# Kernel tuning notes

Measured on AMD Instinct MI355X. Metric: run time of the kernel, lower is better.

## Reference

```python
import jax, jax.numpy as jnp
import numpy as np

N = 50000   # nodes
E = 640000  # edges
D_IN = 128
D_OUT = 128
EPS = 1e-5


def _layer_norm(x, gamma, beta):
    mu = jnp.mean(x, axis=-1, keepdims=True)
    var = jnp.mean(jnp.square(x - mu), axis=-1, keepdims=True)
    return (x - mu) * jax.lax.rsqrt(var + EPS) * gamma + beta


def _sage_conv(x, src, dst, w_l, b_l, w_r):
    # PyG SAGEConv (aggr='mean', root_weight=True, normalize=False):
    #   out = lin_l(mean_{j in N(i)} x_j) + lin_r(x_i)
    msgs = x[src]                                             # [E, D]
    agg = jax.ops.segment_sum(msgs, dst, num_segments=N)      # [N, D]
    cnt = jax.ops.segment_sum(jnp.ones((E,), x.dtype), dst, num_segments=N)
    mean = agg / jnp.maximum(cnt, 1.0)[:, None]
    return mean @ w_l.T + b_l + x @ w_r.T


def setup_inputs() -> dict:
    key = jax.random.key(0)
    ks = jax.random.split(key, 12)
    s_in = 1.0 / np.sqrt(D_IN)
    s_out = 1.0 / np.sqrt(D_OUT)
    return {
        "x": jax.random.normal(ks[0], (N, D_IN), jnp.float32),
        "edges": jax.random.randint(ks[1], (2, E), 0, N),
        "dp_w": jax.random.uniform(ks[2], (D_OUT, D_IN), jnp.float32, -s_in, s_in),
        "dp_b": jnp.zeros((D_OUT,), jnp.float32),
        "sc_w": jax.random.uniform(ks[3], (D_OUT, D_IN), jnp.float32, -s_in, s_in),
        "sc_b": jnp.zeros((D_OUT,), jnp.float32),
        "g1_lw": jax.random.uniform(ks[4], (D_OUT, D_OUT), jnp.float32, -s_out, s_out),
        "g1_lb": jnp.zeros((D_OUT,), jnp.float32),
        "g1_rw": jax.random.uniform(ks[5], (D_OUT, D_OUT), jnp.float32, -s_out, s_out),
        "n1_g": jnp.ones((D_OUT,), jnp.float32),
        "n1_b": jnp.zeros((D_OUT,), jnp.float32),
        "g2_lw": jax.random.uniform(ks[6], (D_OUT, D_OUT), jnp.float32, -s_out, s_out),
        "g2_lb": jnp.zeros((D_OUT,), jnp.float32),
        "g2_rw": jax.random.uniform(ks[7], (D_OUT, D_OUT), jnp.float32, -s_out, s_out),
        "n2_g": jnp.ones((D_OUT,), jnp.float32),
        "n2_b": jnp.zeros((D_OUT,), jnp.float32),
    }


def reference(x, edges, dp_w, dp_b, sc_w, sc_b, g1_lw, g1_lb, g1_rw, n1_g, n1_b,
              g2_lw, g2_lb, g2_rw, n2_g, n2_b):
    gelu = lambda v: jax.nn.gelu(v, approximate=False)
    src, dst = edges[0], edges[1]
    shortcut = x @ sc_w.T + sc_b
    h = gelu(x @ dp_w.T + dp_b)
    h = _sage_conv(h, src, dst, g1_lw, g1_lb, g1_rw)
    h = gelu(_layer_norm(h, n1_g, n1_b))
    h = _sage_conv(h, src, dst, g2_lw, g2_lb, g2_rw)
    h = _layer_norm(h, n2_g, n2_b)
    return gelu(h + shortcut)
```

## Files before the change

kernel.cpp:

```cpp
#include <hip/hip_runtime.h>
#include <hip/hip_bf16.h>
#include <math.h>

#define D 128
#define WS 136
#define FS 132
#define PB 128

typedef __attribute__((ext_vector_type(8))) short bf16x8;
typedef __attribute__((ext_vector_type(4))) float f32x4;

__device__ __forceinline__ unsigned short f2bf(float f){
  return (unsigned short)((__float_as_uint(f) + 0x8000u) >> 16);
}
__device__ __forceinline__ float bf2f(unsigned short h){
  return __uint_as_float(((unsigned)h) << 16);
}
__device__ __forceinline__ float bf2f_lo(unsigned v){
  return __uint_as_float(v << 16);
}
__device__ __forceinline__ float bf2f_hi(unsigned v){
  return __uint_as_float(v & 0xFFFF0000u);
}
__device__ __forceinline__ float gelu_fast(float v){
  float u = v * v;
  float arg = v * (1.5957691216f + 0.0713548163f * u);
  arg = fminf(arg, 60.0f);
  float e = __expf(arg);
  return v * e * __builtin_amdgcn_rcpf(e + 1.0f);
}

__global__ __launch_bounds__(256) void k_prepcnt(const float* s0, const float* s1,
    const float* s2, const float* s3, const float* s4, const float* s5,
    unsigned short* dst, const int* __restrict__ edst, int* __restrict__ cnt,
    int E, int nbuck, int epb){
  __shared__ int hist[512];
  if (blockIdx.x < 48){
    int gt = blockIdx.x * 256 + threadIdx.x;
    int m = gt >> 11;
    int r = gt & 2047;
    int f = r >> 6, lane = r & 63;
    int t = f & 7, kk = f >> 3;
    int row = t * 16 + (lane & 15);
    int col = kk * 32 + (lane >> 4) * 8;
    const float* src;
    if (m == 0) src = s0; else if (m == 1) src = s1; else if (m == 2) src = s2;
    else if (m == 3) src = s3; else if (m == 4) src = s4; else src = s5;
    src += row * 128 + col;
    float4 a = *(const float4*)src;
    float4 bb = *(const float4*)(src + 4);
    bf16x8 o;
    o[0] = (short)f2bf(a.x);  o[1] = (short)f2bf(a.y);
    o[2] = (short)f2bf(a.z);  o[3] = (short)f2bf(a.w);
    o[4] = (short)f2bf(bb.x); o[5] = (short)f2bf(bb.y);
    o[6] = (short)f2bf(bb.z); o[7] = (short)f2bf(bb.w);
    int pair = m >> 1, half = m & 1;
    *(bf16x8*)(dst + (size_t)pair * 32768 + (((size_t)f * 2 + half) * 64 + lane) * 8) = o;
    return;
  }
  int blk = blockIdx.x - 48;
  for (int b = threadIdx.x; b < nbuck; b += 256) hist[b] = 0;
  __syncthreads();
  int start = blk * epb;
  int end = min(E, start + epb);
  for (int e = start + threadIdx.x; e < end; e += 256)
    atomicAdd(&hist[edst[e] >> 7], 1);
  __syncthreads();
  for (int b = threadIdx.x; b < nbuck; b += 256) cnt[blk * nbuck + b] = hist[b];
}

__global__ __launch_bounds__(128) void k_scanA(const int* __restrict__ cnt,
    int* __restrict__ offs_rel, int* __restrict__ tot, int nbuck){
  __shared__ int sm[128];
  int b = blockIdx.x, t = threadIdx.x;
  int v = cnt[t * nbuck + b];
  sm[t] = v; __syncthreads();
  for (int ofs = 1; ofs < 128; ofs <<= 1){
    int u = (t >= ofs) ? sm[t - ofs] : 0;
    __syncthreads();
    sm[t] += u;
    __syncthreads();
  }
  offs_rel[t * nbuck + b] = sm[t] - v;
  if (t == 127) tot[b] = sm[127];
}

__global__ __launch_bounds__(256) void k_pscatter(const int* __restrict__ esrc,
    const int* __restrict__ edst, const int* __restrict__ offs_rel,
    const int* __restrict__ tot, unsigned* __restrict__ ebuf,
    int E, int nbuck, int epb){
  __shared__ int stot[512];
  __shared__ int loff[512];
  for (int b = threadIdx.x; b < nbuck; b += 256) stot[b] = tot[b];
  __syncthreads();
  for (int b = threadIdx.x; b < nbuck; b += 256){
    int s = 0;
    for (int j = 0; j < b; j++) s += stot[j];
    loff[b] = s + offs_rel[blockIdx.x * nbuck + b];
  }
  __syncthreads();
  int start = blockIdx.x * epb;
  int end = min(E, start + epb);
  for (int e = start + threadIdx.x; e < end; e += 256){
    int s = esrc[e], d = edst[e];
    int b = d >> 7;
    int pos = atomicAdd(&loff[b], 1);
    ebuf[pos] = (unsigned)s | ((unsigned)(d & 127) << 16);
  }
}

__global__ __launch_bounds__(256) void k_csrin(
    const unsigned* __restrict__ ebuf, const int* __restrict__ tot,
    int* __restrict__ off, int* __restrict__ csr,
    const float* __restrict__ x, const unsigned short* __restrict__ wp,
    const float* __restrict__ scb, const float* __restrict__ dpb,
    unsigned short* __restrict__ sbuf, unsigned short* __restrict__ hbuf,
    int N, int E, int nbuck){
  __shared__ int cnt[128], pref[128], curs[128];
  __shared__ int stot[512], red[256];
  __shared__ unsigned short tile[64 * WS];
  int tid = threadIdx.x;
  if ((int)blockIdx.x < nbuck){
    int b = blockIdx.x;
    for (int j = tid; j < nbuck; j += 256) stot[j] = tot[j];
    __syncthreads();
    int part = 0;
    for (int j = tid; j < b; j += 256) part += stot[j];
    red[tid] = part;
    __syncthreads();
    for (int ofs = 128; ofs > 0; ofs >>= 1){
      if (tid < ofs) red[tid] += red[tid + ofs];
      __syncthreads();
    }
    int start = red[0];
    int end = start + stot[b];
    if (tid < 128) cnt[tid] = 0;
    __syncthreads();
    for (int e = start + tid; e < end; e += 256)
      atomicAdd(&cnt[ebuf[e] >> 16], 1);
    __syncthreads();
    if (tid < 128) pref[tid] = cnt[tid];
    __syncthreads();
    for (int ofs = 1; ofs < 128; ofs <<= 1){
      int v = 0;
      if (tid < 128 && tid >= ofs) v = pref[tid - ofs];
      __syncthreads();
      if (tid < 128) pref[tid] += v;
      __syncthreads();
    }
    if (tid < 128){
      int ex = pref[tid] - cnt[tid];
      curs[tid] = ex;
      int node = b * 128 + tid;
      if (node < N) off[node] = start + ex;
    }
    if (b == 0 && tid == 0) off[N] = E;
    __syncthreads();
    for (int e = start + tid; e < end; e += 256){
      unsigned u = ebuf[e];
      int d = u >> 16;
      int p = atomicAdd(&curs[d], 1);
      csr[start + p] = (int)(u & 0xFFFFu);
    }
    return;
  }
  int bx = blockIdx.x - nbuck;
  int w = tid >> 6, lane = tid & 63, quad = lane >> 4, l16 = lane & 15;
  int nbb = bx * 64;
  int nb = nbb + w * 16;
  int arow = min(nb + l16, N - 1);
  f32x4 acc[2][8];
  #pragma unroll
  for (int m = 0; m < 2; m++)
    #pragma unroll
    for (int t = 0; t < 8; t++) acc[m][t] = (f32x4){0.f, 0.f, 0.f, 0.f};
  #pragma unroll
  for (int kk = 0; kk < 4; kk++){
    const float* xp = x + (size_t)arow * D + kk * 32 + quad * 8;
    float4 xa = *(const float4*)xp;
    float4 xb = *(const float4*)(xp + 4);
    bf16x8 a;
    a[0] = (short)f2bf(xa.x); a[1] = (short)f2bf(xa.y);
    a[2] = (short)f2bf(xa.z); a[3] = (short)f2bf(xa.w);
    a[4] = (short)f2bf(xb.x); a[5] = (short)f2bf(xb.y);
    a[6] = (short)f2bf(xb.z); a[7] = (short)f2bf(xb.w);
    #pragma unroll
    for (int t = 0; t < 8; t++){
      size_t fo = (((size_t)(kk * 8 + t) * 2) * 64 + lane) * 8;
      bf16x8 b0 = *(const bf16x8*)(wp + fo);
      bf16x8 b1 = *(const bf16x8*)(wp + fo + 512);
      acc[0][t] = __builtin_amdgcn_mfma_f32_16x16x32_bf16(a, b0, acc[0][t], 0, 0, 0);
      acc[1][t] = __builtin_amdgcn_mfma_f32_16x16x32_bf16(a, b1, acc[1][t], 0, 0, 0);
    }
  }
  #pragma unroll
  for (int m = 0; m < 2; m++){
    const float* bias = m ? dpb : scb;
    #pragma unroll
    for (int t = 0; t < 8; t++){
      float bv = bias[t * 16 + l16];
      #pragma unroll
      for (int r = 0; r < 4; r++){
        int nl = w * 16 + quad * 4 + r;
        float v = acc[m][t][r] + bv;
        if (m) v = gelu_fast(v);
        tile[nl * WS + t * 16 + l16] = f2bf(v);
      }
    }
    __syncthreads();
    unsigned short* dst = m ? hbuf : sbuf;
    #pragma unroll
    for (int i = 0; i < 4; i++){
      int c = tid + 256 * i;
      int nl = c >> 4, j = c & 15;
      int node = nbb + nl;
      if (node < N)
        *(bf16x8*)(dst + (size_t)node * D + j * 8) = *(const bf16x8*)(tile + nl * WS + j * 8);
    }
    __syncthreads();
  }
}

__global__ __launch_bounds__(256) void k_gall(
    const unsigned short* __restrict__ hin,
    const int* __restrict__ off, const int* __restrict__ csr,
    const unsigned short* __restrict__ wp,
    const float* __restrict__ lb, const float* __restrict__ gamma,
    const float* __restrict__ beta,
    const unsigned short* __restrict__ sbuf,
    unsigned short* __restrict__ hout, float* __restrict__ fout, int N, int mode){
  extern __shared__ char smraw[];
  unsigned short* mtile = (unsigned short*)smraw;
  unsigned short* stile = (unsigned short*)smraw;
  float* ftile = (float*)smraw;
  int tid = threadIdx.x;
  int nbb = blockIdx.x * 64;
  {
    int q = tid >> 4, l16g = tid & 15;
    int n0 = nbb + q * 4;
    int s0 = off[min(n0 + 0, N)];
    int s1 = off[min(n0 + 1, N)];
    int s2 = off[min(n0 + 2, N)];
    int s3 = off[min(n0 + 3, N)];
    int s4 = off[min(n0 + 4, N)];
    float aT[8], a1[8], a2[8], a3[8];
    #pragma unroll
    for (int c = 0; c < 8; c++){ aT[c] = 0.f; a1[c] = 0.f; a2[c] = 0.f; a3[c] = 0.f; }
    if (s4 > s0){
      int nn[8];
      #pragma unroll
      for (int i = 0; i < 8; i++) nn[i] = csr[min(s0 + i, s4 - 1)];
      for (int e = s0; e < s4; e += 8){
        uint4 v[8];
        #pragma unroll
        for (int i = 0; i < 8; i++)
          v[i] = *(const uint4*)(hin + (size_t)nn[i] * D + l16g * 8);
        #pragma unroll
        for (int i = 0; i < 8; i++) nn[i] = csr[min(e + 8 + i, s4 - 1)];
        #pragma unroll
        for (int i = 0; i < 8; i++){
          int ei = e + i;
          float mT = (ei < s4) ? 1.f : 0.f;
          float m1 = (ei >= s1) ? mT : 0.f;
          float m2 = (ei >= s2) ? mT : 0.f;
          float m3 = (ei >= s3) ? mT : 0.f;
          float fv[8];
          fv[0] = bf2f_lo(v[i].x); fv[1] = bf2f_hi(v[i].x);
          fv[2] = bf2f_lo(v[i].y); fv[3] = bf2f_hi(v[i].y);
          fv[4] = bf2f_lo(v[i].z); fv[5] = bf2f_hi(v[i].z);
          fv[6] = bf2f_lo(v[i].w); fv[7] = bf2f_hi(v[i].w);
          #pragma unroll
          for (int c = 0; c < 8; c++){
            aT[c] += mT * fv[c];
            a1[c] += m1 * fv[c];
            a2[c] += m2 * fv[c];
            a3[c] += m3 * fv[c];
          }
        }
      }
    }
    float i0 = 1.f / (float)max(s1 - s0, 1);
    float i1 = 1.f / (float)max(s2 - s1, 1);
    float i2 = 1.f / (float)max(s3 - s2, 1);
    float i3 = 1.f / (float)max(s4 - s3, 1);
    bf16x8 o0, o1, o2, o3;
    #pragma unroll
    for (int c = 0; c < 8; c++){
      o0[c] = (short)f2bf((aT[c] - a1[c]) * i0);
      o1[c] = (short)f2bf((a1[c] - a2[c]) * i1);
      o2[c] = (short)f2bf((a2[c] - a3[c]) * i2);
      o3[c] = (short)f2bf(a3[c] * i3);
    }
    *(bf16x8*)(mtile + (q * 4 + 0) * WS + l16g * 8) = o0;
    *(bf16x8*)(mtile + (q * 4 + 1) * WS + l16g * 8) = o1;
    *(bf16x8*)(mtile + (q * 4 + 2) * WS + l16g * 8) = o2;
    *(bf16x8*)(mtile + (q * 4 + 3) * WS + l16g * 8) = o3;
  }
  __syncthreads();
  int w = tid >> 6, lane = tid & 63, quad = lane >> 4, l16 = lane & 15;
  int nb = nbb + w * 16;
  int arow = min(nb + l16, N - 1);
  int mrow = w * 16 + l16;
  bf16x8 am[4], ah[4];
  #pragma unroll
  for (int kk = 0; kk < 4; kk++){
    am[kk] = *(const bf16x8*)(mtile + mrow * WS + kk * 32 + quad * 8);
    ah[kk] = *(const bf16x8*)(hin + (size_t)arow * D + kk * 32 + quad * 8);
  }
  f32x4 acc[8];
  #pragma unroll
  for (int t = 0; t < 8; t++) acc[t] = (f32x4){0.f, 0.f, 0.f, 0.f};
  #pragma unroll
  for (int kk = 0; kk < 4; kk++){
    #pragma unroll
    for (int t = 0; t < 8; t++){
      size_t fo = (((size_t)(kk * 8 + t) * 2) * 64 + lane) * 8;
      bf16x8 bl = *(const bf16x8*)(wp + fo);
      bf16x8 br = *(const bf16x8*)(wp + fo + 512);
      acc[t] = __builtin_amdgcn_mfma_f32_16x16x32_bf16(am[kk], bl, acc[t], 0, 0, 0);
      acc[t] = __builtin_amdgcn_mfma_f32_16x16x32_bf16(ah[kk], br, acc[t], 0, 0, 0);
    }
  }
  float lbv[8], gv[8], bv[8];
  #pragma unroll
  for (int t = 0; t < 8; t++){
    lbv[t] = lb[t * 16 + l16];
    gv[t] = gamma[t * 16 + l16];
    bv[t] = beta[t * 16 + l16];
  }
  float mu[4], rs[4];
  #pragma unroll
  for (int r = 0; r < 4; r++){
    float s = 0.f, qq = 0.f;
    #pragma unroll
    for (int t = 0; t < 8; t++){
      float v = acc[t][r] + lbv[t];
      acc[t][r] = v;
      s += v; qq += v * v;
    }
    s += __shfl_xor(s, 1); qq += __shfl_xor(qq, 1);
    s += __shfl_xor(s, 2); qq += __shfl_xor(qq, 2);
    s += __shfl_xor(s, 4); qq += __shfl_xor(qq, 4);
    s += __shfl_xor(s, 8); qq += __shfl_xor(qq, 8);
    float m_ = s * (1.f / 128.f);
    mu[r] = m_;
    rs[r] = rsqrtf(qq * (1.f / 128.f) - m_ * m_ + 1e-5f);
  }
  __syncthreads();
  if (mode == 0){
    #pragma unroll
    for (int t = 0; t < 8; t++)
      #pragma unroll
      for (int r = 0; r < 4; r++){
        int nl = w * 16 + quad * 4 + r;
        float v = (acc[t][r] - mu[r]) * rs[r] * gv[t] + bv[t];
        stile[nl * WS + t * 16 + l16] = f2bf(gelu_fast(v));
      }
    __syncthreads();
    #pragma unroll
    for (int i = 0; i < 4; i++){
      int c = tid + 256 * i;
      int nl = c >> 4, j = c & 15;
      int node = nbb + nl;
      if (node < N)
        *(bf16x8*)(hout + (size_t)node * D + j * 8) = *(const bf16x8*)(stile + nl * WS + j * 8);
    }
  } else {
    #pragma unroll
    for (int i = 0; i < 4; i++){
      int c = tid + 256 * i;
      int nl = c >> 4, j = c & 15;
      int node = nbb + nl;
      bf16x8 v = (bf16x8){0,0,0,0,0,0,0,0};
      if (node < N) v = *(const bf16x8*)(sbuf + (size_t)node * D + j * 8);
      *(bf16x8*)(stile + nl * WS + j * 8) = v;
    }
    __syncthreads();
    float sc[8][4];
    #pragma unroll
    for (int t = 0; t < 8; t++)
      #pragma unroll
      for (int r = 0; r < 4; r++){
        int nl = w * 16 + quad * 4 + r;
        sc[t][r] = bf2f(stile[nl * WS + t * 16 + l16]);
      }
    __syncthreads();
    #pragma unroll
    for (int t = 0; t < 8; t++)
      #pragma unroll
      for (int r = 0; r < 4; r++){
        int nl = w * 16 + quad * 4 + r;
        float v = (acc[t][r] - mu[r]) * rs[r] * gv[t] + bv[t];
        ftile[nl * FS + t * 16 + l16] = gelu_fast(v + sc[t][r]);
      }
    __syncthreads();
    #pragma unroll
    for (int i = 0; i < 8; i++){
      int c = tid + 256 * i;
      int nl = c >> 5, j = c & 31;
      int node = nbb + nl;
      if (node < N)
        *(float4*)(fout + (size_t)node * D + j * 4) = *(const float4*)(ftile + nl * FS + j * 4);
    }
  }
}

extern "C" void kernel_launch(void* const* d_in, const int* in_sizes, int n_in,
                              void* d_out, int out_size, void* d_ws, size_t ws_size,
                              hipStream_t stream){
  const float* x     = (const float*)d_in[0];
  const int*   edges = (const int*)d_in[1];
  const float* dp_w  = (const float*)d_in[2];
  const float* dp_b  = (const float*)d_in[3];
  const float* sc_w  = (const float*)d_in[4];
  const float* sc_b  = (const float*)d_in[5];
  const float* g1_lw = (const float*)d_in[6];
  const float* g1_lb = (const float*)d_in[7];
  const float* g1_rw = (const float*)d_in[8];
  const float* n1_g  = (const float*)d_in[9];
  const float* n1_b  = (const float*)d_in[10];
  const float* g2_lw = (const float*)d_in[11];
  const float* g2_lb = (const float*)d_in[12];
  const float* g2_rw = (const float*)d_in[13];
  const float* n2_g  = (const float*)d_in[14];
  const float* n2_b  = (const float*)d_in[15];

  const int N = in_sizes[0] / D;
  const int E = in_sizes[1] / 2;
  const int* esrc = edges;
  const int* edst = edges + E;
  const int nbuck = (N + 127) >> 7;
  const int epb = (E + PB - 1) / PB;

  char* base = (char*)d_ws;
  size_t cur = 0;
  auto carve = [&](size_t b) -> char* {
    char* p = base + cur;
    cur = (cur + b + 255) & ~(size_t)255;
    return p;
  };
  unsigned* ebuf  = (unsigned*)carve((size_t)E * 4);
  int* cnt        = (int*)carve((size_t)PB * nbuck * 4);
  int* offs_rel   = (int*)carve((size_t)PB * nbuck * 4);
  int* tot        = (int*)carve((size_t)nbuck * 4);
  int* off        = (int*)carve((size_t)(N + 1) * 4);
  int* csr        = (int*)carve((size_t)E * 4);
  unsigned short* wb    = (unsigned short*)carve((size_t)3 * 32768 * 2);
  unsigned short* hbuf  = (unsigned short*)carve((size_t)N * D * 2);
  unsigned short* h1buf = (unsigned short*)carve((size_t)N * D * 2);
  unsigned short* sbuf  = (unsigned short*)carve((size_t)N * D * 2);

  unsigned short* wp0 = wb;
  unsigned short* wp1 = wb + 32768;
  unsigned short* wp2 = wb + 2 * 32768;

  float* out = (float*)d_out;

  k_prepcnt<<<48 + PB, 256, 0, stream>>>(sc_w, dp_w, g1_lw, g1_rw, g2_lw, g2_rw,
                                         wb, edst, cnt, E, nbuck, epb);
  k_scanA<<<nbuck, 128, 0, stream>>>(cnt, offs_rel, tot, nbuck);
  k_pscatter<<<PB, 256, 0, stream>>>(esrc, edst, offs_rel, tot, ebuf, E, nbuck, epb);

  const int nin = (N + 63) / 64;
  k_csrin<<<nbuck + nin, 256, 0, stream>>>(ebuf, tot, off, csr,
                                           x, wp0, sc_b, dp_b, sbuf, hbuf,
                                           N, E, nbuck);

  k_gall<<<nin, 256, 17408, stream>>>(hbuf, off, csr, wp1, g1_lb, n1_g, n1_b,
                                      nullptr, h1buf, nullptr, N, 0);
  k_gall<<<nin, 256, 33792, stream>>>(h1buf, off, csr, wp2, g2_lb, n2_g, n2_b,
                                      sbuf, nullptr, out, N, 1);
}
```

Before: 231.5 us.

## Split fused gather+GEMM into separate per-node gather and GEMM kernels

Splits the fused neighbor-mean aggregation and MFMA GEMM kernel into two kernels. The gather now assigns 16 lanes per node, one node per group, with no masked 4-node accumulation. It writes the mean to a new global bf16 buffer that the GEMM kernel then reads. This removes the redundant four-accumulator masked work and the load imbalance of the fused gather, and adds parallelism. The cost is an extra global round trip of an N×128 bf16 buffer and two extra kernel launches.

```diff
diff --git a/kernel.cpp b/kernel.cpp
--- a/kernel.cpp
+++ b/kernel.cpp
@@ -221,90 +221,71 @@
   }
 }
 
-__global__ __launch_bounds__(256) void k_gall(
+__global__ __launch_bounds__(256) void k_gather(
     const unsigned short* __restrict__ hin,
     const int* __restrict__ off, const int* __restrict__ csr,
+    unsigned short* __restrict__ mout, int N){
+  int tid = threadIdx.x;
+  int node = blockIdx.x * 16 + (tid >> 4);
+  int l16 = tid & 15;
+  if (node >= N) return;
+  int s0 = off[node], s1 = off[node + 1];
+  float acc[8];
+  #pragma unroll
+  for (int c = 0; c < 8; c++) acc[c] = 0.f;
+  if (s1 > s0){
+    const unsigned short* hp = hin + l16 * 8;
+    int nn[8];
+    #pragma unroll
+    for (int i = 0; i < 8; i++) nn[i] = csr[min(s0 + i, s1 - 1)];
+    for (int e = s0; e < s1; e += 8){
+      uint4 v[8];
+      #pragma unroll
+      for (int i = 0; i < 8; i++)
+        v[i] = *(const uint4*)(hp + (size_t)nn[i] * D);
+      #pragma unroll
+      for (int i = 0; i < 8; i++) nn[i] = csr[min(e + 8 + i, s1 - 1)];
+      #pragma unroll
+      for (int i = 0; i < 8; i++){
+        float m = (e + i < s1) ? 1.f : 0.f;
+        acc[0] += m * bf2f_lo(v[i].x);
+        acc[1] += m * bf2f_hi(v[i].x);
+        acc[2] += m * bf2f_lo(v[i].y);
+        acc[3] += m * bf2f_hi(v[i].y);
+        acc[4] += m * bf2f_lo(v[i].z);
+        acc[5] += m * bf2f_hi(v[i].z);
+        acc[6] += m * bf2f_lo(v[i].w);
+        acc[7] += m * bf2f_hi(v[i].w);
+      }
+    }
+  }
+  float inv = 1.f / (float)max(s1 - s0, 1);
+  bf16x8 o;
+  #pragma unroll
+  for (int c = 0; c < 8; c++) o[c] = (short)f2bf(acc[c] * inv);
+  *(bf16x8*)(mout + (size_t)node * D + l16 * 8) = o;
+}
+
+__global__ __launch_bounds__(256) void k_gemm(
+    const unsigned short* __restrict__ hin,
+    const unsigned short* __restrict__ mbuf,
     const unsigned short* __restrict__ wp,
     const float* __restrict__ lb, const float* __restrict__ gamma,
     const float* __restrict__ beta,
     const unsigned short* __restrict__ sbuf,
     unsigned short* __restrict__ hout, float* __restrict__ fout, int N, int mode){
   extern __shared__ char smraw[];
-  unsigned short* mtile = (unsigned short*)smraw;
   unsigned short* stile = (unsigned short*)smraw;
   float* ftile = (float*)smraw;
   int tid = threadIdx.x;
   int nbb = blockIdx.x * 64;
-  {
-    int q = tid >> 4, l16g = tid & 15;
-    int n0 = nbb + q * 4;
-    int s0 = off[min(n0 + 0, N)];
-    int s1 = off[min(n0 + 1, N)];
-    int s2 = off[min(n0 + 2, N)];
-    int s3 = off[min(n0 + 3, N)];
-    int s4 = off[min(n0 + 4, N)];
-    float aT[8], a1[8], a2[8], a3[8];
-    #pragma unroll
-    for (int c = 0; c < 8; c++){ aT[c] = 0.f; a1[c] = 0.f; a2[c] = 0.f; a3[c] = 0.f; }
-    if (s4 > s0){
-      int nn[8];
-      #pragma unroll
-      for (int i = 0; i < 8; i++) nn[i] = csr[min(s0 + i, s4 - 1)];
-      for (int e = s0; e < s4; e += 8){
-        uint4 v[8];
-        #pragma unroll
-        for (int i = 0; i < 8; i++)
-          v[i] = *(const uint4*)(hin + (size_t)nn[i] * D + l16g * 8);
-        #pragma unroll
-        for (int i = 0; i < 8; i++) nn[i] = csr[min(e + 8 + i, s4 - 1)];
-        #pragma unroll
-        for (int i = 0; i < 8; i++){
-          int ei = e + i;
-          float mT = (ei < s4) ? 1.f : 0.f;
-          float m1 = (ei >= s1) ? mT : 0.f;
-          float m2 = (ei >= s2) ? mT : 0.f;
-          float m3 = (ei >= s3) ? mT : 0.f;
-          float fv[8];
-          fv[0] = bf2f_lo(v[i].x); fv[1] = bf2f_hi(v[i].x);
-          fv[2] = bf2f_lo(v[i].y); fv[3] = bf2f_hi(v[i].y);
-          fv[4] = bf2f_lo(v[i].z); fv[5] = bf2f_hi(v[i].z);
-          fv[6] = bf2f_lo(v[i].w); fv[7] = bf2f_hi(v[i].w);
-          #pragma unroll
-          for (int c = 0; c < 8; c++){
-            aT[c] += mT * fv[c];
-            a1[c] += m1 * fv[c];
-            a2[c] += m2 * fv[c];
-            a3[c] += m3 * fv[c];
-          }
-        }
-      }
-    }
-    float i0 = 1.f / (float)max(s1 - s0, 1);
-    float i1 = 1.f / (float)max(s2 - s1, 1);
-    float i2 = 1.f / (float)max(s3 - s2, 1);
-    float i3 = 1.f / (float)max(s4 - s3, 1);
-    bf16x8 o0, o1, o2, o3;
-    #pragma unroll
-    for (int c = 0; c < 8; c++){
-      o0[c] = (short)f2bf((aT[c] - a1[c]) * i0);
-      o1[c] = (short)f2bf((a1[c] - a2[c]) * i1);
-      o2[c] = (short)f2bf((a2[c] - a3[c]) * i2);
-      o3[c] = (short)f2bf(a3[c] * i3);
-    }
-    *(bf16x8*)(mtile + (q * 4 + 0) * WS + l16g * 8) = o0;
-    *(bf16x8*)(mtile + (q * 4 + 1) * WS + l16g * 8) = o1;
-    *(bf16x8*)(mtile + (q * 4 + 2) * WS + l16g * 8) = o2;
-    *(bf16x8*)(mtile + (q * 4 + 3) * WS + l16g * 8) = o3;
-  }
-  __syncthreads();
   int w = tid >> 6, lane = tid & 63, quad = lane >> 4, l16 = lane & 15;
   int nb = nbb + w * 16;
   int arow = min(nb + l16, N - 1);
-  int mrow = w * 16 + l16;
   bf16x8 am[4], ah[4];
   #pragma unroll
   for (int kk = 0; kk < 4; kk++){
-    am[kk] = *(const bf16x8*)(mtile + mrow * WS + kk * 32 + quad * 8);
+    am[kk] = *(const bf16x8*)(mbuf + (size_t)arow * D + kk * 32 + quad * 8);
     ah[kk] = *(const bf16x8*)(hin + (size_t)arow * D + kk * 32 + quad * 8);
   }
   f32x4 acc[8];
@@ -346,7 +327,6 @@
     mu[r] = m_;
     rs[r] = rsqrtf(qq * (1.f / 128.f) - m_ * m_ + 1e-5f);
   }
-  __syncthreads();
   if (mode == 0){
     #pragma unroll
     for (int t = 0; t < 8; t++)
@@ -449,6 +429,7 @@
   unsigned short* hbuf  = (unsigned short*)carve((size_t)N * D * 2);
   unsigned short* h1buf = (unsigned short*)carve((size_t)N * D * 2);
   unsigned short* sbuf  = (unsigned short*)carve((size_t)N * D * 2);
+  unsigned short* mbuf  = (unsigned short*)carve((size_t)N * D * 2);
 
   unsigned short* wp0 = wb;
   unsigned short* wp1 = wb + 32768;
@@ -466,8 +447,11 @@
                                            x, wp0, sc_b, dp_b, sbuf, hbuf,
                                            N, E, nbuck);
 
-  k_gall<<<nin, 256, 17408, stream>>>(hbuf, off, csr, wp1, g1_lb, n1_g, n1_b,
+  const int ngat = (N + 15) / 16;
+  k_gather<<<ngat, 256, 0, stream>>>(hbuf, off, csr, mbuf, N);
+  k_gemm<<<nin, 256, 17408, stream>>>(hbuf, mbuf, wp1, g1_lb, n1_g, n1_b,
                                       nullptr, h1buf, nullptr, N, 0);
-  k_gall<<<nin, 256, 33792, stream>>>(h1buf, off, csr, wp2, g2_lb, n2_g, n2_b,
+  k_gather<<<ngat, 256, 0, stream>>>(h1buf, off, csr, mbuf, N);
+  k_gemm<<<nin, 256, 33792, stream>>>(h1buf, mbuf, wp2, g2_lb, n2_g, n2_b,
                                       sbuf, nullptr, out, N, 1);
 }
```

Result: slower. 238.3 us (+2.9%).
